# Kernel optimization log

Measured on AMD Instinct MI355X. Metric: run time of the kernel, lower is better.

## Reference

```python
import math
import jax, jax.numpy as jnp
import numpy as np

# gpt-oss config constants (layer_idx=1 -> sliding_window disabled)
HID = 2880
N_HEADS = 64
N_KV = 8
D_HEAD = 64
GROUPS = N_HEADS // N_KV  # 8 query heads per kv head
SLIDING_WINDOW = 0        # layer_idx % 2 == 1 -> full causal attention
SM_SCALE = 1.0 / math.sqrt(D_HEAD)
EPS = 1e-5

ROPE_BASE = 150000.0
INIT_CTX = 4096
SCALING = 32.0
NTK_ALPHA = 1.0
NTK_BETA = 32.0


def _rope_cos_sin(num_tokens: int):
    """YaRN-scaled RoPE tables, fp32, positions 0..num_tokens-1 (offset=0, no cache)."""
    d_half = D_HEAD // 2
    freq = ROPE_BASE ** (np.arange(0, D_HEAD, 2, dtype=np.float64) / D_HEAD)
    concentration = 0.1 * math.log(SCALING) + 1.0
    low = d_half * math.log(INIT_CTX / (NTK_BETA * 2 * math.pi)) / math.log(ROPE_BASE)
    high = d_half * math.log(INIT_CTX / (NTK_ALPHA * 2 * math.pi)) / math.log(ROPE_BASE)
    interpolation = 1.0 / (SCALING * freq)
    extrapolation = 1.0 / freq
    ramp = (np.arange(d_half, dtype=np.float64) - low) / (high - low)
    mask = 1.0 - np.clip(ramp, 0.0, 1.0)
    inv_freq = interpolation * (1.0 - mask) + extrapolation * mask
    t = np.arange(num_tokens, dtype=np.float64)
    freqs = np.outer(t, inv_freq)  # [S, d_half]
    cos = (np.cos(freqs) * concentration).astype(np.float32)
    sin = (np.sin(freqs) * concentration).astype(np.float32)
    return jnp.asarray(cos), jnp.asarray(sin)


def _rotate(x, cos, sin):
    # x: [B, S, nh, D]; cos/sin: [S, D/2]
    c = cos[None, :, None, :]
    s = sin[None, :, None, :]
    x1, x2 = jnp.split(x, 2, axis=-1)
    return jnp.concatenate([x1 * c - x2 * s, x2 * c + x1 * s], axis=-1)


def setup_inputs() -> dict:
    key = jax.random.key(0)
    ks = jax.random.split(key, 5)
    B, S = 1, 1536
    x = jax.random.normal(ks[0], (B, S, HID), dtype=jnp.float32)
    sinks = jax.random.normal(ks[1], (N_HEADS,), dtype=jnp.float32) * 0.5
    norm_scale = jnp.ones((HID,), dtype=jnp.float32)
    qkv_dim = D_HEAD * (N_HEADS + 2 * N_KV)  # 5120
    qkv_w = jax.random.normal(ks[2], (qkv_dim, HID), dtype=jnp.float32) * 0.02
    qkv_b = jnp.zeros((qkv_dim,), dtype=jnp.float32)
    out_w = jax.random.normal(ks[3], (HID, N_HEADS * D_HEAD), dtype=jnp.float32) * 0.02
    out_b = jnp.zeros((HID,), dtype=jnp.float32)
    return {"x": x, "sinks": sinks, "norm_scale": norm_scale,
            "qkv_w": qkv_w, "qkv_b": qkv_b, "out_w": out_w, "out_b": out_b}


def reference(x, sinks, norm_scale, qkv_w, qkv_b, out_w, out_b):
    B, S, _ = x.shape
    # RMSNorm (fp32)
    t = x * jax.lax.rsqrt(jnp.mean(x * x, axis=-1, keepdims=True) + EPS) * norm_scale
    # fused QKV projection
    qkv = jnp.einsum('bsd,od->bso', t, qkv_w) + qkv_b
    q, k, v = jnp.split(qkv, [N_HEADS * D_HEAD, (N_HEADS + N_KV) * D_HEAD], axis=-1)
    q = q.reshape(B, S, N_HEADS, D_HEAD)
    k = k.reshape(B, S, N_KV, D_HEAD)
    v = v.reshape(B, S, N_KV, D_HEAD)
    # RoPE (offset = 0, no cache)
    cos, sin = _rope_cos_sin(S)
    q = _rotate(q, cos, sin)
    k = _rotate(k, cos, sin)
    # GQA: head h = g*N_KV + kv
    q = q.reshape(B, S, GROUPS, N_KV, D_HEAD)
    scores = jnp.einsum('bqgkd,bskd->bgkqs', q, k) * SM_SCALE  # [B,G,KV,S,S]
    i = jnp.arange(S)[:, None]
    j = jnp.arange(S)[None, :]
    allowed = j <= i  # causal
    if SLIDING_WINDOW > 0:
        allowed = allowed & (i - j < SLIDING_WINDOW)
    scores = jnp.where(allowed[None, None, None, :, :], scores, -1e30)
    # softmax with learned per-head sink logit in the denominator
    sink = sinks.reshape(GROUPS, N_KV)[None, :, :, None]  # [1,G,KV,1]
    m = jnp.maximum(jnp.max(scores, axis=-1), sink)       # [B,G,KV,S]
    p = jnp.exp(scores - m[..., None])
    denom = jnp.sum(p, axis=-1) + jnp.exp(sink - m)
    attn = p / denom[..., None]
    o = jnp.einsum('bgkqs,bskd->bqgkd', attn, v).reshape(B, S, N_HEADS * D_HEAD)
    y = jnp.einsum('bse,oe->bso', o, out_w) + out_b
    return x + y
```

## Files before the change

### kernel.cpp

```cpp
#include <hip/hip_runtime.h>
#include <hip/hip_bf16.h>
#include <math.h>

typedef unsigned short u16;
typedef __attribute__((ext_vector_type(8))) short bf16x8;
typedef __attribute__((ext_vector_type(4))) float f32x4;
typedef __attribute__((ext_vector_type(4))) u16 u16x4;

#define S_LEN   1536
#define HID     2880
#define NH      64
#define NKV     8
#define DH      64
#define QKV_N   5120
#define QDIM    4096
#define KVDIM   512
#define SMSCALE 0.125f
#define EPSV    1e-5f

__device__ __forceinline__ float b2f(u16 u) {
    unsigned int v = ((unsigned int)u) << 16;
    float f; __builtin_memcpy(&f, &v, 4); return f;
}
__device__ __forceinline__ u16 f2b(float f) {
    __hip_bfloat16 h = __float2bfloat16(f);
    return *reinterpret_cast<u16*>(&h);
}
__device__ __forceinline__ void gld16(const u16* g, u16* l) {
    __builtin_amdgcn_global_load_lds(
        (const __attribute__((address_space(1))) unsigned int*)g,
        (__attribute__((address_space(3))) unsigned int*)l, 16, 0, 0);
}
#define WAIT_VM6()   __builtin_amdgcn_s_waitcnt(0xF76)
#define WAIT_VM4()   __builtin_amdgcn_s_waitcnt(0xF74)
#define WAIT_VM0()   __builtin_amdgcn_s_waitcnt(0xF70)
#define WAIT_LGKM0() __builtin_amdgcn_s_waitcnt(0xC07F)

__global__ __launch_bounds__(256) void conv_bf16_kernel(
    const float* __restrict__ src, u16* __restrict__ dst, int n4)
{
    int i = blockIdx.x * 256 + threadIdx.x;
    if (i >= n4) return;
    float4 v = ((const float4*)src)[i];
    u16x4 o;
    o.x = f2b(v.x); o.y = f2b(v.y); o.z = f2b(v.z); o.w = f2b(v.w);
    ((u16x4*)dst)[i] = o;
}

__global__ __launch_bounds__(256) void rmsnorm_kernel(
    const float* __restrict__ x, const float* __restrict__ ns, u16* __restrict__ t)
{
    const int s = blockIdx.x;
    const int tid = threadIdx.x;
    const float* xr = x + (size_t)s * HID;
    float ss = 0.f;
    for (int i = tid; i < HID; i += 256) { float v = xr[i]; ss += v * v; }
    for (int off = 32; off > 0; off >>= 1) ss += __shfl_down(ss, off);
    __shared__ float red[4];
    if ((tid & 63) == 0) red[tid >> 6] = ss;
    __syncthreads();
    float tot = red[0] + red[1] + red[2] + red[3];
    float scale = rsqrtf(tot / (float)HID + EPSV);
    u16* tr = t + (size_t)s * HID;
    for (int i = tid; i < HID; i += 256)
        tr[i] = f2b(xr[i] * scale * ns[i]);
}

__global__ __launch_bounds__(256) void rope_table_kernel(float* __restrict__ cosT, float* __restrict__ sinT)
{
    int idx = blockIdx.x * 256 + threadIdx.x;
    if (idx >= S_LEN * 32) return;
    int s = idx >> 5, i = idx & 31;
    const double PI2 = 6.283185307179586476925286766559;
    double base = 150000.0;
    double freq = pow(base, (double)(2 * i) / 64.0);
    double conc = 0.1 * log(32.0) + 1.0;
    double low  = 32.0 * log(4096.0 / (32.0 * PI2)) / log(base);
    double high = 32.0 * log(4096.0 / (1.0  * PI2)) / log(base);
    double interp = 1.0 / (32.0 * freq);
    double extrap = 1.0 / freq;
    double ramp = ((double)i - low) / (high - low);
    double msk = 1.0 - fmin(fmax(ramp, 0.0), 1.0);
    double invf = interp * (1.0 - msk) + extrap * msk;
    double ang = (double)s * invf;
    cosT[idx] = (float)(cos(ang) * conc);
    sinT[idx] = (float)(sin(ang) * conc);
}

__global__ __launch_bounds__(512, 2) void gemm_bt_8p_kernel(
    const u16* __restrict__ A, const u16* __restrict__ B,
    u16* __restrict__ Cp, u16* __restrict__ Cp2,
    int M, int N, int K, int it0, int it1, int ntm, int ntn)
{
    extern __shared__ __align__(16) u16 smem[];
    u16* sAp = smem;
    u16* sBp = smem + 32768;

    const int tid  = threadIdx.x;
    const int wave = tid >> 6, lane = tid & 63;
    const int quad = lane >> 4, l16 = lane & 15;
    const int wm = wave >> 2, wn = wave & 3;

    const int nwg  = gridDim.x;
    const int cpx  = nwg >> 3;
    const int flat = blockIdx.x;
    const int swz  = (flat & 7) * cpx + (flat >> 3);
    const int tpz  = ntm * ntn;
    const int z    = swz / tpz;
    const int rem  = swz - z * tpz;
    const int nt   = rem / ntm;
    const int mt   = rem - nt * ntm;
    const int bm = mt * 256, bn = nt * 256;
    const int niter = z ? it1 : it0;
    const int kb    = z ? (it0 + (z - 1) * it1) * 64 : 0;
    u16* C = (z < 2) ? (Cp + (size_t)z * M * N) : Cp2;

    const int r2  = tid >> 2;
    const int ks8 = (tid & 3) * 8;
    const u16* gA0 = A + (size_t)(bm + r2) * K + kb + ks8;
    const u16* gA1 = gA0 + (size_t)128 * K;
    int brA = bn + r2;       if (brA > N - 1) brA = N - 1;
    int brB = bn + 128 + r2; if (brB > N - 1) brB = N - 1;
    const u16* gB0 = B + (size_t)brA * K + kb + ks8;
    const u16* gB1 = B + (size_t)brB * K + kb + ks8;
    const int sw = wave * 512;

    f32x4 acc[8][4];
    #pragma unroll
    for (int i = 0; i < 8; i++)
        #pragma unroll
        for (int j = 0; j < 4; j++) acc[i][j] = (f32x4){0.f, 0.f, 0.f, 0.f};

    auto stA = [&](int c, int kh, int t) {
        u16* d = sAp + (((c << 1) | kh) << 13);
        const int koff = t * 64 + kh * 32;
        gld16(gA0 + koff, d + sw);
        gld16(gA1 + koff, d + 4096 + sw);
    };
    auto stB = [&](int c, int kh, int t) {
        u16* d = sBp + (((c << 1) | kh) << 13);
        const int koff = t * 64 + kh * 32;
        gld16(gB0 + koff, d + sw);
        gld16(gB1 + koff, d + 4096 + sw);
    };

    bf16x8 bv[4];
    const int arow = wm * 128 + l16;
    const int brow = wn * 64 + l16;
    auto rdB = [&](int c, int ks) {
        const u16* p = sBp + (((c << 1) | ks) << 13) + brow * 32 + quad * 8;
        #pragma unroll
        for (int nf = 0; nf < 4; nf++) bv[nf] = *(const bf16x8*)(p + nf * 16 * 32);
    };
    auto mmph = [&](int c, int ks, int mh) {
        const u16* p = sAp + (((c << 1) | ks) << 13) + (arow + mh * 64) * 32 + quad * 8;
        bf16x8 av[4];
        #pragma unroll
        for (int mf = 0; mf < 4; mf++) av[mf] = *(const bf16x8*)(p + mf * 16 * 32);
        __builtin_amdgcn_s_setprio(1);
        #pragma unroll
        for (int mf = 0; mf < 4; mf++)
            #pragma unroll
            for (int nf = 0; nf < 4; nf++)
                acc[mh * 4 + mf][nf] = __builtin_amdgcn_mfma_f32_16x16x32_bf16(
                    av[mf], bv[nf], acc[mh * 4 + mf][nf], 0, 0, 0);
        __builtin_amdgcn_s_setprio(0);
    };

    stA(0, 0, 0); stB(0, 0, 0); stA(0, 1, 0); stB(0, 1, 0);

    for (int t = 0; t < niter - 1; ++t) {
        const int c = t & 1;
        stA(c ^ 1, 0, t + 1);
        WAIT_VM6();
        __builtin_amdgcn_s_barrier();
        rdB(c, 0); mmph(c, 0, 0);
        stB(c ^ 1, 0, t + 1);
        mmph(c, 0, 1);
        stA(c ^ 1, 1, t + 1);
        WAIT_VM6();
        __builtin_amdgcn_s_barrier();
        rdB(c, 1); mmph(c, 1, 0);
        stB(c ^ 1, 1, t + 1);
        mmph(c, 1, 1);
    }
    {
        const int c = (niter - 1) & 1;
        WAIT_VM4();
        __builtin_amdgcn_s_barrier();
        rdB(c, 0); mmph(c, 0, 0); mmph(c, 0, 1);
        WAIT_VM0();
        __builtin_amdgcn_s_barrier();
        rdB(c, 1); mmph(c, 1, 0); mmph(c, 1, 1);
    }

    #pragma unroll
    for (int im = 0; im < 8; im++) {
        const int row0 = bm + wm * 128 + im * 16 + quad * 4;
        #pragma unroll
        for (int nf = 0; nf < 4; nf++) {
            const int col = bn + wn * 64 + nf * 16 + l16;
            if (col < N) {
                #pragma unroll
                for (int r = 0; r < 4; r++)
                    C[(size_t)(row0 + r) * N + col] = f2b(acc[im][nf][r]);
            }
        }
    }
}

__global__ __launch_bounds__(256) void rope_apply_kernel(
    const u16* __restrict__ p0, const u16* __restrict__ p1, const float* __restrict__ bias,
    const float* __restrict__ cosT, const float* __restrict__ sinT,
    u16* __restrict__ q_r, u16* __restrict__ k_r, u16* __restrict__ v_r)
{
    int idx = blockIdx.x * 256 + threadIdx.x;
    if (idx >= S_LEN * 80 * 64) return;
    int s  = idx / 5120;
    int rem = idx - s * 5120;
    int hh = rem >> 6;
    int i  = rem & 63;
    const u16* r0p = p0 + (size_t)s * QKV_N;
    const u16* r1p = p1 + (size_t)s * QKV_N;
    #define QKVV(o) (b2f(r0p[o]) + b2f(r1p[o]) + bias[o])
    if (hh < 64) {
        int off = hh * 64, j = i & 31;
        float x1 = QKVV(off + j), x2 = QKVV(off + 32 + j);
        float c = cosT[s * 32 + j], sn = sinT[s * 32 + j];
        float val = (i < 32) ? (x1 * c - x2 * sn) : (x2 * c + x1 * sn);
        q_r[(size_t)s * QDIM + off + i] = f2b(val * SMSCALE);
    } else if (hh < 72) {
        int kh = hh - 64, off = QDIM + kh * 64, j = i & 31;
        float x1 = QKVV(off + j), x2 = QKVV(off + 32 + j);
        float c = cosT[s * 32 + j], sn = sinT[s * 32 + j];
        float val = (i < 32) ? (x1 * c - x2 * sn) : (x2 * c + x1 * sn);
        k_r[(size_t)s * KVDIM + kh * 64 + i] = f2b(val);
    } else {
        int vh = hh - 72, off = QDIM + KVDIM + vh * 64;
        v_r[(size_t)s * KVDIM + vh * 64 + i] = f2b(QKVV(off + i));
    }
    #undef QKVV
}

__global__ __launch_bounds__(256) void vt_kernel(
    const u16* __restrict__ v_r, u16* __restrict__ vt)
{
    __shared__ u16 tile[64][72];
    const int s0 = blockIdx.x * 64;
    const int kvh = blockIdx.y;
    const int tid = threadIdx.x;
    const int r = tid >> 3;
    const int c = (tid & 7) * 8;

    #pragma unroll
    for (int rr = 0; rr < 64; rr += 32) {
        uint4 vv = *(const uint4*)(v_r + (size_t)(s0 + r + rr) * KVDIM + kvh * 64 + c);
        const u16* p = (const u16*)&vv;
        #pragma unroll
        for (int j = 0; j < 8; j++) tile[c + j][r + rr] = p[j];
    }
    __syncthreads();
    #pragma unroll
    for (int rr = 0; rr < 64; rr += 32) {
        uint4 ov;
        u16* p = (u16*)&ov;
        #pragma unroll
        for (int j = 0; j < 8; j++) p[j] = tile[r + rr][c + j];
        *(uint4*)(vt + (size_t)(kvh * 64 + r + rr) * S_LEN + s0 + c) = ov;
    }
}

__global__ __launch_bounds__(256) void attn_kernel(
    const u16* __restrict__ q_r, const u16* __restrict__ k_r, const u16* __restrict__ vt,
    const float* __restrict__ sinks, u16* __restrict__ o)
{
    __shared__ __align__(16) u16 sK[2][64 * 72];
    __shared__ __align__(16) u16 sVt[2][64 * 72];
    __shared__ __align__(16) u16 sP[4 * 16 * 72];

    const int bx = blockIdx.x, h = blockIdx.y;
    const int kvh = h & 7;
    const int tid = threadIdx.x, wave = tid >> 6, lane = tid & 63;
    const int quad = lane >> 4, l16 = lane & 15;
    const int srow = tid >> 3;
    const int scol = (tid & 7) * 8;
    u16* sPw = sP + wave * 16 * 72;
    const float sinkv = sinks[h];

    uint4 kreg0, kreg1, vreg0, vreg1;
    const u16* kbase = k_r + (size_t)srow * KVDIM + kvh * 64 + scol;
    const u16* vbase = vt + (size_t)(kvh * 64 + srow) * S_LEN + scol;

    auto issue = [&](int j0) {
        kreg0 = *(const uint4*)(kbase + (size_t)j0 * KVDIM);
        kreg1 = *(const uint4*)(kbase + (size_t)(j0 + 32) * KVDIM);
        vreg0 = *(const uint4*)(vbase + j0);
        vreg1 = *(const uint4*)(vbase + (size_t)32 * S_LEN + j0);
    };
    auto lwrite = [&](int c) {
        *(uint4*)(&sK[c][srow * 72 + scol])        = kreg0;
        *(uint4*)(&sK[c][(srow + 32) * 72 + scol]) = kreg1;
        *(uint4*)(&sVt[c][srow * 72 + scol])        = vreg0;
        *(uint4*)(&sVt[c][(srow + 32) * 72 + scol]) = vreg1;
    };

    for (int phase = 0; phase < 2; ++phase) {
        const int qt = phase ? (23 - bx) : bx;
        const int q_i = qt * 64 + wave * 16 + l16;
        const u16* qp = q_r + (size_t)q_i * QDIM + h * 64 + quad * 8;
        bf16x8 aq0 = *(const bf16x8*)(qp);
        bf16x8 aq1 = *(const bf16x8*)(qp + 32);

        float m_i = sinkv, l_i = 1.0f;
        f32x4 acc[4];
        #pragma unroll
        for (int dt = 0; dt < 4; dt++) acc[dt] = (f32x4){0.f, 0.f, 0.f, 0.f};

        const int ntile = qt + 1;
        issue(0);
        __syncthreads();

        for (int tt = 0; tt < ntile; ++tt) {
            const int c = tt & 1;
            lwrite(c);
            if (tt + 1 < ntile) issue((tt + 1) * 64);
            WAIT_LGKM0();
            __builtin_amdgcn_s_barrier();

            f32x4 sc[4];
            __builtin_amdgcn_s_setprio(1);
            #pragma unroll
            for (int nt = 0; nt < 4; nt++) {
                const u16* kp = &sK[c][(nt * 16 + l16) * 72 + quad * 8];
                bf16x8 bk0 = *(const bf16x8*)(kp);
                bf16x8 bk1 = *(const bf16x8*)(kp + 32);
                f32x4 s0 = (f32x4){0.f, 0.f, 0.f, 0.f};
                s0 = __builtin_amdgcn_mfma_f32_16x16x32_bf16(bk0, aq0, s0, 0, 0, 0);
                s0 = __builtin_amdgcn_mfma_f32_16x16x32_bf16(bk1, aq1, s0, 0, 0, 0);
                sc[nt] = s0;
            }
            __builtin_amdgcn_s_setprio(0);

            if (tt == qt) {
                #pragma unroll
                for (int nt = 0; nt < 4; nt++)
                    #pragma unroll
                    for (int r = 0; r < 4; r++)
                        if (tt * 64 + nt * 16 + quad * 4 + r > q_i) sc[nt][r] = -INFINITY;
            }

            float vmax = sc[0][0];
            #pragma unroll
            for (int nt = 0; nt < 4; nt++)
                #pragma unroll
                for (int r = 0; r < 4; r++) vmax = fmaxf(vmax, sc[nt][r]);
            vmax = fmaxf(vmax, __shfl_xor(vmax, 16));
            vmax = fmaxf(vmax, __shfl_xor(vmax, 32));
            if (__any(vmax > m_i + 8.0f)) {
                float mnew = fmaxf(m_i, vmax);
                float alpha = __expf(m_i - mnew);
                l_i *= alpha;
                #pragma unroll
                for (int dt = 0; dt < 4; dt++)
                    #pragma unroll
                    for (int r = 0; r < 4; r++) acc[dt][r] *= alpha;
                m_i = mnew;
            }
            float ps = 0.f;
            u16x4 pk[4];
            #pragma unroll
            for (int nt = 0; nt < 4; nt++) {
                #pragma unroll
                for (int r = 0; r < 4; r++) {
                    float p = __expf(sc[nt][r] - m_i);
                    ps += p;
                    pk[nt][r] = f2b(p);
                }
            }
            ps += __shfl_xor(ps, 16);
            ps += __shfl_xor(ps, 32);
            l_i += ps;
            #pragma unroll
            for (int nt = 0; nt < 4; nt++)
                *(u16x4*)(sPw + l16 * 72 + nt * 16 + quad * 4) = pk[nt];
            __threadfence_block();

            bf16x8 ap0 = *(const bf16x8*)(sPw + l16 * 72 + quad * 8);
            bf16x8 ap1 = *(const bf16x8*)(sPw + l16 * 72 + 32 + quad * 8);
            __builtin_amdgcn_s_setprio(1);
            #pragma unroll
            for (int dt = 0; dt < 4; dt++) {
                const u16* vp = &sVt[c][(dt * 16 + l16) * 72 + quad * 8];
                bf16x8 bv0 = *(const bf16x8*)(vp);
                bf16x8 bv1 = *(const bf16x8*)(vp + 32);
                acc[dt] = __builtin_amdgcn_mfma_f32_16x16x32_bf16(bv0, ap0, acc[dt], 0, 0, 0);
                acc[dt] = __builtin_amdgcn_mfma_f32_16x16x32_bf16(bv1, ap1, acc[dt], 0, 0, 0);
            }
            __builtin_amdgcn_s_setprio(0);
        }

        float inv = 1.0f / l_i;
        #pragma unroll
        for (int dt = 0; dt < 4; dt++) {
            u16x4 ov;
            #pragma unroll
            for (int r = 0; r < 4; r++) ov[r] = f2b(acc[dt][r] * inv);
            *(u16x4*)(o + (size_t)q_i * QDIM + h * 64 + dt * 16 + quad * 4) = ov;
        }
    }
}

__global__ __launch_bounds__(256) void final_add_kernel(
    const u16* __restrict__ p0, const u16* __restrict__ p1, const u16* __restrict__ p2,
    const float* __restrict__ bias, const float* __restrict__ x, float* __restrict__ out)
{
    int i = blockIdx.x * 256 + threadIdx.x;
    int base = i * 4;
    int col = base % HID;
    float4 xo = *(const float4*)(x + base);
    float4 bi = *(const float4*)(bias + col);
    u16x4 a = ((const u16x4*)p0)[i];
    u16x4 b = ((const u16x4*)p1)[i];
    u16x4 c = ((const u16x4*)p2)[i];
    float4 r;
    r.x = b2f(a.x) + b2f(b.x) + b2f(c.x) + bi.x + xo.x;
    r.y = b2f(a.y) + b2f(b.y) + b2f(c.y) + bi.y + xo.y;
    r.z = b2f(a.z) + b2f(b.z) + b2f(c.z) + bi.z + xo.z;
    r.w = b2f(a.w) + b2f(b.w) + b2f(c.w) + bi.w + xo.w;
    *(float4*)(out + base) = r;
}

extern "C" void kernel_launch(void* const* d_in, const int* in_sizes, int n_in,
                              void* d_out, int out_size, void* d_ws, size_t ws_size,
                              hipStream_t stream)
{
    const float* x          = (const float*)d_in[0];
    const float* sinks      = (const float*)d_in[1];
    const float* norm_scale = (const float*)d_in[2];
    const float* qkv_w      = (const float*)d_in[3];
    const float* qkv_b      = (const float*)d_in[4];
    const float* out_w      = (const float*)d_in[5];
    const float* out_b      = (const float*)d_in[6];
    float* out = (float*)d_out;

    char* ws = (char*)d_ws;
    u16* t        = (u16*)(ws);
    u16* qkv_w_bf = (u16*)(ws + 8847360);
    u16* qkvp0    = (u16*)(ws + 38338560);
    u16* qkvp1    = (u16*)(ws + 54067200);
    float* cosT   = (float*)(ws + 69795840);
    float* sinT   = (float*)(ws + 69992448);
    u16* k_r      = (u16*)(ws);
    u16* vt       = (u16*)(ws + 1572864);
    u16* q_r      = (u16*)(ws + 3145728);
    u16* o        = (u16*)(ws + 15728640);
    u16* v_r      = (u16*)(ws + 28311552);
    u16* outp0    = (u16*)(ws + 28311552);
    u16* outp1    = (u16*)(ws + 37158912);
    u16* outp2    = (u16*)(ws + 3145728);
    u16* out_w_bf = (u16*)(ws + 46006272);

    static bool lds_attr_set = false;
    if (!lds_attr_set) {
        hipFuncSetAttribute(reinterpret_cast<const void*>(gemm_bt_8p_kernel),
                            hipFuncAttributeMaxDynamicSharedMemorySize, 131072);
        lds_attr_set = true;
    }

    rmsnorm_kernel<<<S_LEN, 256, 0, stream>>>(x, norm_scale, t);
    conv_bf16_kernel<<<(QKV_N * HID / 4 + 255) / 256, 256, 0, stream>>>(qkv_w, qkv_w_bf, QKV_N * HID / 4);
    rope_table_kernel<<<(S_LEN * 32) / 256, 256, 0, stream>>>(cosT, sinT);
    gemm_bt_8p_kernel<<<240, 512, 131072, stream>>>(
        t, qkv_w_bf, qkvp0, qkvp0, S_LEN, QKV_N, HID, 23, 22, 6, 20);
    rope_apply_kernel<<<(S_LEN * 80 * 64) / 256, 256, 0, stream>>>(
        qkvp0, qkvp1, qkv_b, cosT, sinT, q_r, k_r, v_r);
    vt_kernel<<<dim3(S_LEN / 64, NKV), 256, 0, stream>>>(v_r, vt);
    conv_bf16_kernel<<<(HID * QDIM / 4 + 255) / 256, 256, 0, stream>>>(out_w, out_w_bf, HID * QDIM / 4);
    attn_kernel<<<dim3(12, NH), 256, 0, stream>>>(q_r, k_r, vt, sinks, o);
    gemm_bt_8p_kernel<<<216, 512, 131072, stream>>>(
        o, out_w_bf, outp0, outp2, S_LEN, HID, QDIM, 22, 21, 6, 12);
    final_add_kernel<<<S_LEN * HID / 4 / 256, 256, 0, stream>>>(outp0, outp1, outp2, out_b, x, out);
}
```

Before: 331.6 us.

## Process paired causal query tiles concurrently sharing each K/V tile load

Each block used to process two query tiles (bx and 23-bx) in two sequential phases, reloading K/V tiles for each. Now both query tiles are processed in a single pass over the longer tile's K/V range. Each staged K/V tile feeds MFMAs for both query sets whenever the shorter one is still active, which roughly halves K/V global loads and barriers for the short tile. The cost is doubled accumulator and score registers and a larger P buffer in shared memory, which may lower occupancy, plus the extra work runs only under a per-tile branch.

```diff
diff --git a/kernel.cpp b/kernel.cpp
--- a/kernel.cpp
+++ b/kernel.cpp
@@ -276,7 +276,7 @@
 {
     __shared__ __align__(16) u16 sK[2][64 * 72];
     __shared__ __align__(16) u16 sVt[2][64 * 72];
-    __shared__ __align__(16) u16 sP[4 * 16 * 72];
+    __shared__ __align__(16) u16 sP[4][2][16 * 72];
 
     const int bx = blockIdx.x, h = blockIdx.y;
     const int kvh = h & 7;
@@ -284,7 +284,6 @@
     const int quad = lane >> 4, l16 = lane & 15;
     const int srow = tid >> 3;
     const int scol = (tid & 7) * 8;
-    u16* sPw = sP + wave * 16 * 72;
     const float sinkv = sinks[h];
 
     uint4 kreg0, kreg1, vreg0, vreg1;
@@ -304,109 +303,151 @@
         *(uint4*)(&sVt[c][(srow + 32) * 72 + scol]) = vreg1;
     };
 
-    for (int phase = 0; phase < 2; ++phase) {
-        const int qt = phase ? (23 - bx) : bx;
-        const int q_i = qt * 64 + wave * 16 + l16;
-        const u16* qp = q_r + (size_t)q_i * QDIM + h * 64 + quad * 8;
-        bf16x8 aq0 = *(const bf16x8*)(qp);
-        bf16x8 aq1 = *(const bf16x8*)(qp + 32);
-
-        float m_i = sinkv, l_i = 1.0f;
-        f32x4 acc[4];
-        #pragma unroll
-        for (int dt = 0; dt < 4; dt++) acc[dt] = (f32x4){0.f, 0.f, 0.f, 0.f};
-
-        const int ntile = qt + 1;
-        issue(0);
-        __syncthreads();
-
-        for (int tt = 0; tt < ntile; ++tt) {
-            const int c = tt & 1;
-            lwrite(c);
-            if (tt + 1 < ntile) issue((tt + 1) * 64);
-            WAIT_LGKM0();
-            __builtin_amdgcn_s_barrier();
-
-            f32x4 sc[4];
-            __builtin_amdgcn_s_setprio(1);
+    const int qtA = bx, qtB = 23 - bx;
+    const int qiA = qtA * 64 + wave * 16 + l16;
+    const int qiB = qtB * 64 + wave * 16 + l16;
+    const u16* qpA = q_r + (size_t)qiA * QDIM + h * 64 + quad * 8;
+    const u16* qpB = q_r + (size_t)qiB * QDIM + h * 64 + quad * 8;
+    bf16x8 aqA0 = *(const bf16x8*)(qpA);
+    bf16x8 aqA1 = *(const bf16x8*)(qpA + 32);
+    bf16x8 aqB0 = *(const bf16x8*)(qpB);
+    bf16x8 aqB1 = *(const bf16x8*)(qpB + 32);
+
+    float mA = sinkv, lA = 1.0f, mB = sinkv, lB = 1.0f;
+    f32x4 accA[4], accB[4];
+    #pragma unroll
+    for (int dt = 0; dt < 4; dt++) {
+        accA[dt] = (f32x4){0.f, 0.f, 0.f, 0.f};
+        accB[dt] = (f32x4){0.f, 0.f, 0.f, 0.f};
+    }
+    u16* sPA = &sP[wave][0][0];
+    u16* sPB = &sP[wave][1][0];
+
+    auto softmax = [&](f32x4* sc, f32x4* acc, float& m_i, float& l_i, u16* sPq) {
+        float vmax = sc[0][0];
+        #pragma unroll
+        for (int nt = 0; nt < 4; nt++)
             #pragma unroll
-            for (int nt = 0; nt < 4; nt++) {
-                const u16* kp = &sK[c][(nt * 16 + l16) * 72 + quad * 8];
-                bf16x8 bk0 = *(const bf16x8*)(kp);
-                bf16x8 bk1 = *(const bf16x8*)(kp + 32);
-                f32x4 s0 = (f32x4){0.f, 0.f, 0.f, 0.f};
-                s0 = __builtin_amdgcn_mfma_f32_16x16x32_bf16(bk0, aq0, s0, 0, 0, 0);
-                s0 = __builtin_amdgcn_mfma_f32_16x16x32_bf16(bk1, aq1, s0, 0, 0, 0);
-                sc[nt] = s0;
+            for (int r = 0; r < 4; r++) vmax = fmaxf(vmax, sc[nt][r]);
+        vmax = fmaxf(vmax, __shfl_xor(vmax, 16));
+        vmax = fmaxf(vmax, __shfl_xor(vmax, 32));
+        if (__any(vmax > m_i + 8.0f)) {
+            float mnew = fmaxf(m_i, vmax);
+            float alpha = __expf(m_i - mnew);
+            l_i *= alpha;
+            #pragma unroll
+            for (int dt = 0; dt < 4; dt++)
+                #pragma unroll
+                for (int r = 0; r < 4; r++) acc[dt][r] *= alpha;
+            m_i = mnew;
+        }
+        float ps = 0.f;
+        u16x4 pk[4];
+        #pragma unroll
+        for (int nt = 0; nt < 4; nt++) {
+            #pragma unroll
+            for (int r = 0; r < 4; r++) {
+                float p = __expf(sc[nt][r] - m_i);
+                ps += p;
+                pk[nt][r] = f2b(p);
             }
-            __builtin_amdgcn_s_setprio(0);
-
-            if (tt == qt) {
-                #pragma unroll
-                for (int nt = 0; nt < 4; nt++)
-                    #pragma unroll
-                    for (int r = 0; r < 4; r++)
-                        if (tt * 64 + nt * 16 + quad * 4 + r > q_i) sc[nt][r] = -INFINITY;
+        }
+        ps += __shfl_xor(ps, 16);
+        ps += __shfl_xor(ps, 32);
+        l_i += ps;
+        #pragma unroll
+        for (int nt = 0; nt < 4; nt++)
+            *(u16x4*)(sPq + l16 * 72 + nt * 16 + quad * 4) = pk[nt];
+    };
+
+    const int ntile = qtB + 1;
+    issue(0);
+
+    for (int tt = 0; tt < ntile; ++tt) {
+        const int c = tt & 1;
+        lwrite(c);
+        if (tt + 1 < ntile) issue((tt + 1) * 64);
+        WAIT_LGKM0();
+        __builtin_amdgcn_s_barrier();
+        const bool doA = (tt <= qtA);
+
+        f32x4 scA[4], scB[4];
+        __builtin_amdgcn_s_setprio(1);
+        #pragma unroll
+        for (int nt = 0; nt < 4; nt++) {
+            const u16* kp = &sK[c][(nt * 16 + l16) * 72 + quad * 8];
+            bf16x8 bk0 = *(const bf16x8*)(kp);
+            bf16x8 bk1 = *(const bf16x8*)(kp + 32);
+            f32x4 s0 = (f32x4){0.f, 0.f, 0.f, 0.f};
+            s0 = __builtin_amdgcn_mfma_f32_16x16x32_bf16(bk0, aqB0, s0, 0, 0, 0);
+            s0 = __builtin_amdgcn_mfma_f32_16x16x32_bf16(bk1, aqB1, s0, 0, 0, 0);
+            scB[nt] = s0;
+            if (doA) {
+                f32x4 s1 = (f32x4){0.f, 0.f, 0.f, 0.f};
+                s1 = __builtin_amdgcn_mfma_f32_16x16x32_bf16(bk0, aqA0, s1, 0, 0, 0);
+                s1 = __builtin_amdgcn_mfma_f32_16x16x32_bf16(bk1, aqA1, s1, 0, 0, 0);
+                scA[nt] = s1;
             }
-
-            float vmax = sc[0][0];
+        }
+        __builtin_amdgcn_s_setprio(0);
+
+        if (tt == qtB) {
             #pragma unroll
             for (int nt = 0; nt < 4; nt++)
                 #pragma unroll
-                for (int r = 0; r < 4; r++) vmax = fmaxf(vmax, sc[nt][r]);
-            vmax = fmaxf(vmax, __shfl_xor(vmax, 16));
-            vmax = fmaxf(vmax, __shfl_xor(vmax, 32));
-            if (__any(vmax > m_i + 8.0f)) {
-                float mnew = fmaxf(m_i, vmax);
-                float alpha = __expf(m_i - mnew);
-                l_i *= alpha;
-                #pragma unroll
-                for (int dt = 0; dt < 4; dt++)
-                    #pragma unroll
-                    for (int r = 0; r < 4; r++) acc[dt][r] *= alpha;
-                m_i = mnew;
-            }
-            float ps = 0.f;
-            u16x4 pk[4];
-            #pragma unroll
-            for (int nt = 0; nt < 4; nt++) {
-                #pragma unroll
-                for (int r = 0; r < 4; r++) {
-                    float p = __expf(sc[nt][r] - m_i);
-                    ps += p;
-                    pk[nt][r] = f2b(p);
-                }
-            }
-            ps += __shfl_xor(ps, 16);
-            ps += __shfl_xor(ps, 32);
-            l_i += ps;
+                for (int r = 0; r < 4; r++)
+                    if (tt * 64 + nt * 16 + quad * 4 + r > qiB) scB[nt][r] = -INFINITY;
+        }
+        if (doA && tt == qtA) {
             #pragma unroll
             for (int nt = 0; nt < 4; nt++)
-                *(u16x4*)(sPw + l16 * 72 + nt * 16 + quad * 4) = pk[nt];
-            __threadfence_block();
-
-            bf16x8 ap0 = *(const bf16x8*)(sPw + l16 * 72 + quad * 8);
-            bf16x8 ap1 = *(const bf16x8*)(sPw + l16 * 72 + 32 + quad * 8);
-            __builtin_amdgcn_s_setprio(1);
-            #pragma unroll
-            for (int dt = 0; dt < 4; dt++) {
-                const u16* vp = &sVt[c][(dt * 16 + l16) * 72 + quad * 8];
-                bf16x8 bv0 = *(const bf16x8*)(vp);
-                bf16x8 bv1 = *(const bf16x8*)(vp + 32);
-                acc[dt] = __builtin_amdgcn_mfma_f32_16x16x32_bf16(bv0, ap0, acc[dt], 0, 0, 0);
-                acc[dt] = __builtin_amdgcn_mfma_f32_16x16x32_bf16(bv1, ap1, acc[dt], 0, 0, 0);
+                #pragma unroll
+                for (int r = 0; r < 4; r++)
+                    if (tt * 64 + nt * 16 + quad * 4 + r > qiA) scA[nt][r] = -INFINITY;
+        }
+
+        softmax(scB, accB, mB, lB, sPB);
+        if (doA) softmax(scA, accA, mA, lA, sPA);
+        __threadfence_block();
+
+        bf16x8 apB0 = *(const bf16x8*)(sPB + l16 * 72 + quad * 8);
+        bf16x8 apB1 = *(const bf16x8*)(sPB + l16 * 72 + 32 + quad * 8);
+        bf16x8 apA0, apA1;
+        if (doA) {
+            apA0 = *(const bf16x8*)(sPA + l16 * 72 + quad * 8);
+            apA1 = *(const bf16x8*)(sPA + l16 * 72 + 32 + quad * 8);
+        }
+        __builtin_amdgcn_s_setprio(1);
+        #pragma unroll
+        for (int dt = 0; dt < 4; dt++) {
+            const u16* vp = &sVt[c][(dt * 16 + l16) * 72 + quad * 8];
+            bf16x8 bv0 = *(const bf16x8*)(vp);
+            bf16x8 bv1 = *(const bf16x8*)(vp + 32);
+            accB[dt] = __builtin_amdgcn_mfma_f32_16x16x32_bf16(bv0, apB0, accB[dt], 0, 0, 0);
+            accB[dt] = __builtin_amdgcn_mfma_f32_16x16x32_bf16(bv1, apB1, accB[dt], 0, 0, 0);
+            if (doA) {
+                accA[dt] = __builtin_amdgcn_mfma_f32_16x16x32_bf16(bv0, apA0, accA[dt], 0, 0, 0);
+                accA[dt] = __builtin_amdgcn_mfma_f32_16x16x32_bf16(bv1, apA1, accA[dt], 0, 0, 0);
             }
-            __builtin_amdgcn_s_setprio(0);
-        }
-
-        float inv = 1.0f / l_i;
-        #pragma unroll
-        for (int dt = 0; dt < 4; dt++) {
-            u16x4 ov;
-            #pragma unroll
-            for (int r = 0; r < 4; r++) ov[r] = f2b(acc[dt][r] * inv);
-            *(u16x4*)(o + (size_t)q_i * QDIM + h * 64 + dt * 16 + quad * 4) = ov;
-        }
+        }
+        __builtin_amdgcn_s_setprio(0);
+    }
+
+    float invB = 1.0f / lB;
+    #pragma unroll
+    for (int dt = 0; dt < 4; dt++) {
+        u16x4 ov;
+        #pragma unroll
+        for (int r = 0; r < 4; r++) ov[r] = f2b(accB[dt][r] * invB);
+        *(u16x4*)(o + (size_t)qiB * QDIM + h * 64 + dt * 16 + quad * 4) = ov;
+    }
+    float invA = 1.0f / lA;
+    #pragma unroll
+    for (int dt = 0; dt < 4; dt++) {
+        u16x4 ov;
+        #pragma unroll
+        for (int r = 0; r < 4; r++) ov[r] = f2b(accA[dt][r] * invA);
+        *(u16x4*)(o + (size_t)qiA * QDIM + h * 64 + dt * 16 + quad * 4) = ov;
     }
 }
 
```

Result: slower. 352.0 us (+6.2%).
